# Kernel tuning notes

Measured on AMD Instinct MI355X. Metric: run time of the kernel, lower is better.

Reference implementation:

```python
import jax, jax.numpy as jnp
import numpy as np

TEMPERATURE = 1.0
NEG_INF = -1e30  # finite stand-in for -inf: safe for log_softmax and its vjp


def setup_inputs() -> dict:
    key = jax.random.key(0)
    k1, k2 = jax.random.split(key)
    B, M, D = 4096, 3, 256
    tokens = jax.random.normal(k1, (B, M, D), dtype=jnp.float32)
    labels = jax.random.randint(k2, (B,), 0, 32, dtype=jnp.int32)
    return {"tokens": tokens, "labels": labels}


def reference(tokens, labels):
    # tokens: [B, M, D]; labels: [B]
    B, M, D = tokens.shape
    # Pairwise per-modality similarities: sim[i, k, m] = <tokens[i,m], tokens[k,m]>
    sim = jnp.einsum('imd,kmd->ikm', tokens, tokens) / TEMPERATURE
    self_mask = jnp.eye(B, dtype=bool)
    # Original excludes sample i itself from the candidate set; masking with a
    # huge negative logit makes it contribute 0 to the softmax partition.
    sim = jnp.where(self_mask[:, :, None], NEG_INF, sim)
    logp = jax.nn.log_softmax(sim, axis=1)  # softmax over the B-1 other samples

    # Positive pairs: same label, excluding self.
    pos = (labels[:, None] == labels[None, :]) & ~self_mask  # [B, B]
    pos_count = pos.sum(axis=1)                               # [B]
    valid = pos_count > 0                                     # sum(same_label) > 1

    # Mean log-prob over positives, per (sample, modality).
    pos_logp = jnp.einsum('ikm,ik->im', logp, pos.astype(logp.dtype))  # [B, M]
    denom = jnp.maximum(pos_count, 1).astype(logp.dtype)[:, None]
    per = jnp.where(valid[:, None], pos_logp / denom, 0.0)             # [B, M]

    num = valid.sum() * M
    return -per.sum() / num.astype(per.dtype)
```

## Files before the change

### kernel.cpp

```cpp
#include <hip/hip_runtime.h>

#define B_N 4096
#define M_N 3
#define D_N 256
#define LOG2E 1.44269504088896340736f
#define LN2   0.69314718055994530942f
#define C_OFF   64.0f
#define T_CLAMP 112.0f

typedef __bf16 bf16x8 __attribute__((ext_vector_type(8)));
typedef float  f32x4  __attribute__((ext_vector_type(4)));

__device__ __forceinline__ unsigned short f2bf(float f) {
    unsigned int u = __float_as_uint(f);
    u += 0x7FFFu + ((u >> 16) & 1u);
    return (unsigned short)(u >> 16);
}
__device__ __forceinline__ float bf2f(unsigned short h) {
    return __uint_as_float(((unsigned int)h) << 16);
}

__global__ void cvt_kernel(const float* __restrict__ in, unsigned short* __restrict__ out,
                           float* __restrict__ norm2) {
    int idx = blockIdx.x * blockDim.x + threadIdx.x;
    float4 v = reinterpret_cast<const float4*>(in)[idx];
    int i   = idx / 192;
    int rem = idx - i * 192;
    int m   = rem >> 6;
    int d4  = rem & 63;
    ushort4 o;
    o.x = f2bf(v.x); o.y = f2bf(v.y); o.z = f2bf(v.z); o.w = f2bf(v.w);
    reinterpret_cast<ushort4*>(out)[((size_t)m * B_N + i) * 64 + d4] = o;
    float nx = bf2f(o.x), ny = bf2f(o.y), nz = bf2f(o.z), nw = bf2f(o.w);
    float s = nx * nx + ny * ny + nz * nz + nw * nw;
#pragma unroll
    for (int msk = 1; msk < 64; msk <<= 1) s += __shfl_xor(s, msk);
    if ((threadIdx.x & 63) == 0) norm2[m * B_N + i] = s;
}

__global__ __launch_bounds__(256, 3) void main_kernel(
    const unsigned short* __restrict__ tokb, const int* __restrict__ labels,
    float2* __restrict__ partials) {
    int raw = blockIdx.x;
    int bid = (raw & 7) * 96 + (raw >> 3);
    int m  = bid >> 8;
    int ns = (bid >> 5) & 7;
    int rb = bid & 31;
    int i0 = rb * 128;
    int cb = ns * 512;

    int tid  = threadIdx.x;
    int wave = tid >> 6, lane = tid & 63;
    int lr = lane & 15, lk = lane >> 4;
    const unsigned short* tm = tokb + (size_t)m * (B_N * D_N);

    __shared__ __align__(16) char ldsB[2][8192];
    __shared__ int labl[512];
    labl[tid]       = labels[cb + tid];
    labl[tid + 256] = labels[cb + tid + 256];

    int r0 = i0 + wave * 32;
    bf16x8 afrag[2][8];
#pragma unroll
    for (int rt = 0; rt < 2; ++rt) {
        const unsigned short* rp = tm + (size_t)(r0 + rt * 16 + lr) * D_N + lk * 8;
#pragma unroll
        for (int kf = 0; kf < 8; ++kf)
            afrag[rt][kf] = *reinterpret_cast<const bf16x8*>(rp + kf * 32);
    }
    int labr[2][4];
#pragma unroll
    for (int rt = 0; rt < 2; ++rt)
#pragma unroll
        for (int j = 0; j < 4; ++j)
            labr[rt][j] = labels[r0 + rt * 16 + lk * 4 + j];

    float S[2][4] = {{0.f, 0.f, 0.f, 0.f}, {0.f, 0.f, 0.f, 0.f}};
    float P[2][4] = {{0.f, 0.f, 0.f, 0.f}, {0.f, 0.f, 0.f, 0.f}};

    int lc  = tid >> 5;
    int w   = tid & 31;
    int sch = w ^ (lc & 7);
    const unsigned short* sbase = tm + (size_t)(cb + lc) * D_N + sch * 8;

#define COMPUTE(KB, BUF)                                                            \
    {                                                                               \
        int kb_ = (KB);                                                             \
        const char* bp = ldsB[BUF];                                                 \
        int swz = (lr & 7) << 4;                                                    \
        bf16x8 bfrag[8];                                                            \
        _Pragma("unroll")                                                           \
        for (int kf = 0; kf < 8; ++kf)                                              \
            bfrag[kf] = *reinterpret_cast<const bf16x8*>(                           \
                bp + lr * 512 + (((kf * 4 + lk) << 4) ^ swz));                      \
        int labc = labl[kb_ * 16 + lr];                                             \
        f32x4 acc0 = {0.f, 0.f, 0.f, 0.f};                                          \
        f32x4 acc1 = {0.f, 0.f, 0.f, 0.f};                                          \
        _Pragma("unroll")                                                           \
        for (int kf = 0; kf < 8; ++kf) {                                            \
            acc0 = __builtin_amdgcn_mfma_f32_16x16x32_bf16(afrag[0][kf], bfrag[kf], \
                                                           acc0, 0, 0, 0);          \
            acc1 = __builtin_amdgcn_mfma_f32_16x16x32_bf16(afrag[1][kf], bfrag[kf], \
                                                           acc1, 0, 0, 0);          \
        }                                                                           \
        int cg0 = cb + kb_ * 16;                                                    \
        if ((cg0 < r0 + 32) && (cg0 + 16 > r0)) {                                   \
            int colg = cg0 + lr;                                                    \
            _Pragma("unroll")                                                       \
            for (int rt = 0; rt < 2; ++rt) {                                        \
                f32x4 aa = rt ? acc1 : acc0;                                        \
                _Pragma("unroll")                                                   \
                for (int j = 0; j < 4; ++j) {                                       \
                    float s2 = aa[j];                                               \
                    float t = fminf(fmaf(s2, LOG2E, -C_OFF), T_CLAMP);               \
                    float e = __builtin_amdgcn_exp2f(t);                            \
                    int row = r0 + rt * 16 + lk * 4 + j;                            \
                    e = (colg == row) ? 0.f : e;   \
                    S[rt][j] += e;                                                  \
                    P[rt][j] += (labc == labr[rt][j]) ? s2 : 0.f;                   \
                }                                                                   \
            }                                                                       \
        } else {                                                                    \
            _Pragma("unroll")                                                       \
            for (int rt = 0; rt < 2; ++rt) {                                        \
                f32x4 aa = rt ? acc1 : acc0;                                        \
                _Pragma("unroll")                                                   \
                for (int j = 0; j < 4; ++j) {                                       \
                    float s2 = aa[j];                                               \
                    float t = fminf(fmaf(s2, LOG2E, -C_OFF), T_CLAMP);               \
                    S[rt][j] += __builtin_amdgcn_exp2f(t);                          \
                    P[rt][j] += (labc == labr[rt][j]) ? s2 : 0.f;                   \
                }                                                                   \
            }                                                                       \
        }                                                                           \
    }

    {
        bf16x8 t0 = *reinterpret_cast<const bf16x8*>(sbase);
        bf16x8 t1 = *reinterpret_cast<const bf16x8*>(sbase + 8 * D_N);
        *reinterpret_cast<bf16x8*>(&ldsB[0][tid * 16])        = t0;
        *reinterpret_cast<bf16x8*>(&ldsB[0][4096 + tid * 16]) = t1;
    }
    const unsigned short* p1 = sbase + (size_t)(16 * D_N);
    bf16x8 gA0 = *reinterpret_cast<const bf16x8*>(p1);
    bf16x8 gA1 = *reinterpret_cast<const bf16x8*>(p1 + 8 * D_N);

    for (int it = 0; it < 16; ++it) {
        __syncthreads();
        {
            const unsigned short* np =
                sbase + (size_t)((2 * it + 2) & 31) * (16 * D_N);
            bf16x8 gB0 = *reinterpret_cast<const bf16x8*>(np);
            bf16x8 gB1 = *reinterpret_cast<const bf16x8*>(np + 8 * D_N);
            COMPUTE(2 * it, 0);
            *reinterpret_cast<bf16x8*>(&ldsB[1][tid * 16])        = gA0;
            *reinterpret_cast<bf16x8*>(&ldsB[1][4096 + tid * 16]) = gA1;
            __syncthreads();
            const unsigned short* np2 =
                sbase + (size_t)((2 * it + 3) & 31) * (16 * D_N);
            gA0 = *reinterpret_cast<const bf16x8*>(np2);
            gA1 = *reinterpret_cast<const bf16x8*>(np2 + 8 * D_N);
            COMPUTE(2 * it + 1, 1);
            *reinterpret_cast<bf16x8*>(&ldsB[0][tid * 16])        = gB0;
            *reinterpret_cast<bf16x8*>(&ldsB[0][4096 + tid * 16]) = gB1;
        }
    }
#undef COMPUTE

#pragma unroll
    for (int rt = 0; rt < 2; ++rt)
#pragma unroll
        for (int j = 0; j < 4; ++j) {
            float sv = S[rt][j], pv = P[rt][j];
#pragma unroll
            for (int msk = 1; msk < 16; msk <<= 1) {
                sv += __shfl_xor(sv, msk);
                pv += __shfl_xor(pv, msk);
            }
            if (lr == 0) {
                int rl = rt * 16 + lk * 4 + j;
                float2 q; q.x = sv; q.y = pv;
                partials[(size_t)(((m * 32 + rb) * 8 + ns) * 128) + wave * 32 + rl] = q;
            }
        }
}

__global__ void reduce_kernel(const float2* __restrict__ partials,
                              const float* __restrict__ norm2,
                              const int* __restrict__ labels,
                              float* __restrict__ blockpart,
                              int* __restrict__ nvout) {
    __shared__ int h[32];
    int tid = threadIdx.x;
    if (tid < 32) h[tid] = 0;
    __syncthreads();
    for (int i = tid; i < B_N; i += 256) atomicAdd(&h[labels[i]], 1);
    __syncthreads();
    if (blockIdx.x == 0 && tid == 0) {
        int nv = 0;
#pragma unroll
        for (int c = 0; c < 32; ++c) nv += (h[c] >= 2) ? h[c] : 0;
        nvout[0] = nv;
    }
    int gid = blockIdx.x * 256 + tid;
    int m = gid >> 12, i = gid & 4095;
    int rb = i >> 7, r = i & 127;
    const float2* pp = partials + (size_t)(((m * 32 + rb) * 8) * 128) + r;
    float S = 0.f, P = 0.f;
#pragma unroll
    for (int ns = 0; ns < 8; ++ns) {
        float2 q = pp[ns * 128];
        S += q.x; P += q.y;
    }
    P -= norm2[gid];
    int pc = h[labels[i]] - 1;
    float contrib = (pc > 0)
        ? (__builtin_amdgcn_logf(S) + C_OFF) * LN2 - P / (float)pc
        : 0.f;
#pragma unroll
    for (int off = 32; off >= 1; off >>= 1) contrib += __shfl_down(contrib, off);
    __shared__ float w4[4];
    if ((tid & 63) == 0) w4[tid >> 6] = contrib;
    __syncthreads();
    if (tid == 0) blockpart[blockIdx.x] = w4[0] + w4[1] + w4[2] + w4[3];
}

__global__ void final_kernel(const float* __restrict__ blockpart, const int* __restrict__ nv,
                             float* __restrict__ out) {
    int lane = threadIdx.x;
    float s = (lane < 48) ? blockpart[lane] : 0.f;
#pragma unroll
    for (int off = 32; off >= 1; off >>= 1) s += __shfl_down(s, off);
    if (lane == 0) out[0] = s / (float)(nv[0] * M_N);
}

extern "C" void kernel_launch(void* const* d_in, const int* in_sizes, int n_in,
                              void* d_out, int out_size, void* d_ws, size_t ws_size,
                              hipStream_t stream) {
    const float* tokens = (const float*)d_in[0];
    const int*   labels = (const int*)d_in[1];
    float* out = (float*)d_out;

    char* ws = (char*)d_ws;
    int*    nv        = (int*)(ws + 128);
    float*  blockpart = (float*)(ws + 256);
    float*  norm2     = (float*)(ws + 1024);
    float2* partials  = (float2*)(ws + 65536);
    unsigned short* tokb = (unsigned short*)(ws + 1048576);

    cvt_kernel<<<3072, 256, 0, stream>>>(tokens, tokb, norm2);
    main_kernel<<<768, 256, 0, stream>>>(tokb, labels, partials);
    reduce_kernel<<<48, 256, 0, stream>>>(partials, norm2, labels, blockpart, nv);
    final_kernel<<<1, 64, 0, stream>>>(blockpart, nv, out);
}
```

Before: 58.27 us.

## Triple-buffer LDS and prefetch next B fragments into registers during MFMA

Replaces the double-buffered LDS scheme with a three-slot rotation and register double-buffering of the B fragments, so the next tile's LDS reads overlap the current tile's MFMAs and each phase needs only one barrier. Redundant wrap-around global loads at the tail are skipped. Launch bounds drop from 3 to 2 blocks per CU to leave room for the extra fragment registers, which may lower occupancy and hurt latency hiding.

```diff
diff --git a/kernel.cpp b/kernel.cpp
--- a/kernel.cpp
+++ b/kernel.cpp
@@ -38,7 +38,7 @@
     if ((threadIdx.x & 63) == 0) norm2[m * B_N + i] = s;
 }
 
-__global__ __launch_bounds__(256, 3) void main_kernel(
+__global__ __launch_bounds__(256, 2) void main_kernel(
     const unsigned short* __restrict__ tokb, const int* __restrict__ labels,
     float2* __restrict__ partials) {
     int raw = blockIdx.x;
@@ -54,7 +54,7 @@
     int lr = lane & 15, lk = lane >> 4;
     const unsigned short* tm = tokb + (size_t)m * (B_N * D_N);
 
-    __shared__ __align__(16) char ldsB[2][8192];
+    __shared__ __align__(16) char ldsB[3][8192];
     __shared__ int labl[512];
     labl[tid]       = labels[cb + tid];
     labl[tid + 256] = labels[cb + tid + 256];
@@ -82,90 +82,97 @@
     int w   = tid & 31;
     int sch = w ^ (lc & 7);
     const unsigned short* sbase = tm + (size_t)(cb + lc) * D_N + sch * 8;
-
-#define COMPUTE(KB, BUF)                                                            \
-    {                                                                               \
-        int kb_ = (KB);                                                             \
-        const char* bp = ldsB[BUF];                                                 \
-        int swz = (lr & 7) << 4;                                                    \
-        bf16x8 bfrag[8];                                                            \
-        _Pragma("unroll")                                                           \
-        for (int kf = 0; kf < 8; ++kf)                                              \
-            bfrag[kf] = *reinterpret_cast<const bf16x8*>(                           \
-                bp + lr * 512 + (((kf * 4 + lk) << 4) ^ swz));                      \
-        int labc = labl[kb_ * 16 + lr];                                             \
-        f32x4 acc0 = {0.f, 0.f, 0.f, 0.f};                                          \
-        f32x4 acc1 = {0.f, 0.f, 0.f, 0.f};                                          \
-        _Pragma("unroll")                                                           \
-        for (int kf = 0; kf < 8; ++kf) {                                            \
-            acc0 = __builtin_amdgcn_mfma_f32_16x16x32_bf16(afrag[0][kf], bfrag[kf], \
-                                                           acc0, 0, 0, 0);          \
-            acc1 = __builtin_amdgcn_mfma_f32_16x16x32_bf16(afrag[1][kf], bfrag[kf], \
-                                                           acc1, 0, 0, 0);          \
-        }                                                                           \
-        int cg0 = cb + kb_ * 16;                                                    \
-        if ((cg0 < r0 + 32) && (cg0 + 16 > r0)) {                                   \
-            int colg = cg0 + lr;                                                    \
-            _Pragma("unroll")                                                       \
-            for (int rt = 0; rt < 2; ++rt) {                                        \
-                f32x4 aa = rt ? acc1 : acc0;                                        \
-                _Pragma("unroll")                                                   \
-                for (int j = 0; j < 4; ++j) {                                       \
-                    float s2 = aa[j];                                               \
-                    float t = fminf(fmaf(s2, LOG2E, -C_OFF), T_CLAMP);               \
-                    float e = __builtin_amdgcn_exp2f(t);                            \
-                    int row = r0 + rt * 16 + lk * 4 + j;                            \
-                    e = (colg == row) ? 0.f : e;   \
-                    S[rt][j] += e;                                                  \
-                    P[rt][j] += (labc == labr[rt][j]) ? s2 : 0.f;                   \
-                }                                                                   \
-            }                                                                       \
-        } else {                                                                    \
-            _Pragma("unroll")                                                       \
-            for (int rt = 0; rt < 2; ++rt) {                                        \
-                f32x4 aa = rt ? acc1 : acc0;                                        \
-                _Pragma("unroll")                                                   \
-                for (int j = 0; j < 4; ++j) {                                       \
-                    float s2 = aa[j];                                               \
-                    float t = fminf(fmaf(s2, LOG2E, -C_OFF), T_CLAMP);               \
-                    S[rt][j] += __builtin_amdgcn_exp2f(t);                          \
-                    P[rt][j] += (labc == labr[rt][j]) ? s2 : 0.f;                   \
-                }                                                                   \
-            }                                                                       \
-        }                                                                           \
-    }
+    int swz = (lr & 7) << 4;
 
     {
-        bf16x8 t0 = *reinterpret_cast<const bf16x8*>(sbase);
-        bf16x8 t1 = *reinterpret_cast<const bf16x8*>(sbase + 8 * D_N);
-        *reinterpret_cast<bf16x8*>(&ldsB[0][tid * 16])        = t0;
-        *reinterpret_cast<bf16x8*>(&ldsB[0][4096 + tid * 16]) = t1;
-    }
-    const unsigned short* p1 = sbase + (size_t)(16 * D_N);
-    bf16x8 gA0 = *reinterpret_cast<const bf16x8*>(p1);
-    bf16x8 gA1 = *reinterpret_cast<const bf16x8*>(p1 + 8 * D_N);
+        bf16x8 a0 = *reinterpret_cast<const bf16x8*>(sbase);
+        bf16x8 a1 = *reinterpret_cast<const bf16x8*>(sbase + 8 * D_N);
+        bf16x8 b0 = *reinterpret_cast<const bf16x8*>(sbase + 16 * D_N);
+        bf16x8 b1 = *reinterpret_cast<const bf16x8*>(sbase + 24 * D_N);
+        *reinterpret_cast<bf16x8*>(&ldsB[0][tid * 16])        = a0;
+        *reinterpret_cast<bf16x8*>(&ldsB[0][4096 + tid * 16]) = a1;
+        *reinterpret_cast<bf16x8*>(&ldsB[1][tid * 16])        = b0;
+        *reinterpret_cast<bf16x8*>(&ldsB[1][4096 + tid * 16]) = b1;
+    }
+    __syncthreads();
+
+    char* pc = ldsB[0];
+    char* pn = ldsB[1];
+    char* ps = ldsB[2];
+
+    bf16x8 bfA[8], bfB[8];
+#pragma unroll
+    for (int kf = 0; kf < 8; ++kf)
+        bfA[kf] = *reinterpret_cast<const bf16x8*>(pc + lr * 512 + (((kf * 4 + lk) << 4) ^ swz));
+
+#define PHASE(KB, BFC, BFN)                                                          \
+    {                                                                                \
+        int kb_ = (KB);                                                              \
+        bf16x8 nt0, nt1;                                                             \
+        if (kb_ < 30) {                \
+            const unsigned short* np = sbase + (size_t)(kb_ + 2) * (16 * D_N);       \
+            nt0 = *reinterpret_cast<const bf16x8*>(np);                              \
+            nt1 = *reinterpret_cast<const bf16x8*>(np + 8 * D_N);                    \
+        }                                                                            \
+        f32x4 acc0 = {0.f, 0.f, 0.f, 0.f};                                           \
+        f32x4 acc1 = {0.f, 0.f, 0.f, 0.f};                                           \
+        _Pragma("unroll")                                                            \
+        for (int kf = 0; kf < 8; ++kf) {                                             \
+            acc0 = __builtin_amdgcn_mfma_f32_16x16x32_bf16(afrag[0][kf], BFC[kf],    \
+                                                           acc0, 0, 0, 0);           \
+            acc1 = __builtin_amdgcn_mfma_f32_16x16x32_bf16(afrag[1][kf], BFC[kf],    \
+                                                           acc1, 0, 0, 0);           \
+        }                                                                            \
+        if (kb_ < 31) {      \
+            _Pragma("unroll")                                                        \
+            for (int kf = 0; kf < 8; ++kf)                                           \
+                BFN[kf] = *reinterpret_cast<const bf16x8*>(                          \
+                    pn + lr * 512 + (((kf * 4 + lk) << 4) ^ swz));                   \
+        }                                                                            \
+        int labc = labl[kb_ * 16 + lr];                                              \
+        int cg0 = cb + kb_ * 16;                                                     \
+        if ((cg0 < r0 + 32) && (cg0 + 16 > r0)) {                                    \
+            int colg = cg0 + lr;                                                     \
+            _Pragma("unroll")                                                        \
+            for (int rt = 0; rt < 2; ++rt) {                                         \
+                f32x4 aa = rt ? acc1 : acc0;                                         \
+                _Pragma("unroll")                                                    \
+                for (int j = 0; j < 4; ++j) {                                        \
+                    float s2 = aa[j];                                                \
+                    float t = fminf(fmaf(s2, LOG2E, -C_OFF), T_CLAMP);                \
+                    float e = __builtin_amdgcn_exp2f(t);                             \
+                    int row = r0 + rt * 16 + lk * 4 + j;                             \
+                    e = (colg == row) ? 0.f : e;                                     \
+                    S[rt][j] += e;                                                   \
+                    P[rt][j] += (labc == labr[rt][j]) ? s2 : 0.f;                    \
+                }                                                                    \
+            }                                                                        \
+        } else {                                                                     \
+            _Pragma("unroll")                                                        \
+            for (int rt = 0; rt < 2; ++rt) {                                         \
+                f32x4 aa = rt ? acc1 : acc0;                                         \
+                _Pragma("unroll")                                                    \
+                for (int j = 0; j < 4; ++j) {                                        \
+                    float s2 = aa[j];                                                \
+                    float t = fminf(fmaf(s2, LOG2E, -C_OFF), T_CLAMP);                \
+                    S[rt][j] += __builtin_amdgcn_exp2f(t);                           \
+                    P[rt][j] += (labc == labr[rt][j]) ? s2 : 0.f;                    \
+                }                                                                    \
+            }                                                                        \
+        }                                                                            \
+        if (kb_ < 30) {                                         \
+            *reinterpret_cast<bf16x8*>(ps + tid * 16)        = nt0;                  \
+            *reinterpret_cast<bf16x8*>(ps + 4096 + tid * 16) = nt1;                  \
+        }                                                                            \
+        __syncthreads();                                                             \
+        char* tmp_ = pc; pc = pn; pn = ps; ps = tmp_;                                \
+    }
 
     for (int it = 0; it < 16; ++it) {
-        __syncthreads();
-        {
-            const unsigned short* np =
-                sbase + (size_t)((2 * it + 2) & 31) * (16 * D_N);
-            bf16x8 gB0 = *reinterpret_cast<const bf16x8*>(np);
-            bf16x8 gB1 = *reinterpret_cast<const bf16x8*>(np + 8 * D_N);
-            COMPUTE(2 * it, 0);
-            *reinterpret_cast<bf16x8*>(&ldsB[1][tid * 16])        = gA0;
-            *reinterpret_cast<bf16x8*>(&ldsB[1][4096 + tid * 16]) = gA1;
-            __syncthreads();
-            const unsigned short* np2 =
-                sbase + (size_t)((2 * it + 3) & 31) * (16 * D_N);
-            gA0 = *reinterpret_cast<const bf16x8*>(np2);
-            gA1 = *reinterpret_cast<const bf16x8*>(np2 + 8 * D_N);
-            COMPUTE(2 * it + 1, 1);
-            *reinterpret_cast<bf16x8*>(&ldsB[0][tid * 16])        = gB0;
-            *reinterpret_cast<bf16x8*>(&ldsB[0][4096 + tid * 16]) = gB1;
-        }
-    }
-#undef COMPUTE
+        PHASE(2 * it,     bfA, bfB);
+        PHASE(2 * it + 1, bfB, bfA);
+    }
+#undef PHASE
 
 #pragma unroll
     for (int rt = 0; rt < 2; ++rt)
```

Result: faster. 54.89 us (-5.8%).

## Exploit Gram matrix symmetry by computing only upper-triangular tiles

Applied to the files above, without the earlier changes.

Each (modality, 128x128 block-pair) tile in the upper triangle is now computed once. Its exp-sums and positive-similarity sums feed both the row samples and, for off-diagonal tiles, the column samples through per-column shared-memory reductions. Results are accumulated with global atomics into a zeroed per-sample buffer, replacing the partials array, so the reduce kernel reads a single value per row. This roughly halves the MFMA and exp work, at the cost of extra column shuffles, LDS traffic, atomics and a memset.

```diff
diff --git a/kernel.cpp b/kernel.cpp
--- a/kernel.cpp
+++ b/kernel.cpp
@@ -40,14 +40,16 @@
 
 __global__ __launch_bounds__(256, 3) void main_kernel(
     const unsigned short* __restrict__ tokb, const int* __restrict__ labels,
-    float2* __restrict__ partials) {
+    float* __restrict__ gacc) {
     int raw = blockIdx.x;
-    int bid = (raw & 7) * 96 + (raw >> 3);
-    int m  = bid >> 8;
-    int ns = (bid >> 5) & 7;
-    int rb = bid & 31;
-    int i0 = rb * 128;
-    int cb = ns * 512;
+    int bid = (raw & 7) * 198 + (raw >> 3);
+    int m    = bid / 528;
+    int beta = bid - m * 528;
+    int b = 0;
+    while ((b + 1) * (b + 2) / 2 <= beta) ++b;
+    int a = beta - (b * (b + 1)) / 2;
+    bool offd = (a != b);
+    int cb = b * 128;
 
     int tid  = threadIdx.x;
     int wave = tid >> 6, lane = tid & 63;
@@ -55,11 +57,11 @@
     const unsigned short* tm = tokb + (size_t)m * (B_N * D_N);
 
     __shared__ __align__(16) char ldsB[2][8192];
-    __shared__ int labl[512];
-    labl[tid]       = labels[cb + tid];
-    labl[tid + 256] = labels[cb + tid + 256];
-
-    int r0 = i0 + wave * 32;
+    __shared__ int labl[128];
+    __shared__ float colbuf[4][8][16][2];
+    if (tid < 128) labl[tid] = labels[cb + tid];
+
+    int r0 = a * 128 + wave * 32;
     bf16x8 afrag[2][8];
 #pragma unroll
     for (int rt = 0; rt < 2; ++rt) {
@@ -83,17 +85,30 @@
     int sch = w ^ (lc & 7);
     const unsigned short* sbase = tm + (size_t)(cb + lc) * D_N + sch * 8;
 
-#define COMPUTE(KB, BUF)                                                            \
+    {
+        bf16x8 t0 = *reinterpret_cast<const bf16x8*>(sbase);
+        bf16x8 t1 = *reinterpret_cast<const bf16x8*>(sbase + 8 * D_N);
+        *reinterpret_cast<bf16x8*>(&ldsB[0][tid * 16])        = t0;
+        *reinterpret_cast<bf16x8*>(&ldsB[0][4096 + tid * 16]) = t1;
+    }
+
+#define PHASE(KB)                                                                   \
     {                                                                               \
-        int kb_ = (KB);                                                             \
-        const char* bp = ldsB[BUF];                                                 \
+        __syncthreads();       \
+        bf16x8 nt0, nt1;                                                            \
+        if (KB < 7) {                                                               \
+            const unsigned short* np = sbase + (size_t)(KB + 1) * (16 * D_N);       \
+            nt0 = *reinterpret_cast<const bf16x8*>(np);                             \
+            nt1 = *reinterpret_cast<const bf16x8*>(np + 8 * D_N);                   \
+        }                                                                           \
+        const char* bp = ldsB[KB & 1];                                              \
         int swz = (lr & 7) << 4;                                                    \
         bf16x8 bfrag[8];                                                            \
         _Pragma("unroll")                                                           \
         for (int kf = 0; kf < 8; ++kf)                                              \
             bfrag[kf] = *reinterpret_cast<const bf16x8*>(                           \
                 bp + lr * 512 + (((kf * 4 + lk) << 4) ^ swz));                      \
-        int labc = labl[kb_ * 16 + lr];                                             \
+        int labc = labl[KB * 16 + lr];                                              \
         f32x4 acc0 = {0.f, 0.f, 0.f, 0.f};                                          \
         f32x4 acc1 = {0.f, 0.f, 0.f, 0.f};                                          \
         _Pragma("unroll")                                                           \
@@ -103,8 +118,9 @@
             acc1 = __builtin_amdgcn_mfma_f32_16x16x32_bf16(afrag[1][kf], bfrag[kf], \
                                                            acc1, 0, 0, 0);          \
         }                                                                           \
-        int cg0 = cb + kb_ * 16;                                                    \
-        if ((cg0 < r0 + 32) && (cg0 + 16 > r0)) {                                   \
+        float cs = 0.f, cp = 0.f;                                                   \
+        int cg0 = cb + KB * 16;                                                     \
+        if ((cg0 < r0 + 32) && (cg0 + 16 > r0)) {          \
             int colg = cg0 + lr;                                                    \
             _Pragma("unroll")                                                       \
             for (int rt = 0; rt < 2; ++rt) {                                        \
@@ -116,8 +132,9 @@
                     float e = __builtin_amdgcn_exp2f(t);                            \
                     int row = r0 + rt * 16 + lk * 4 + j;                            \
                     e = (colg == row) ? 0.f : e;   \
-                    S[rt][j] += e;                                                  \
-                    P[rt][j] += (labc == labr[rt][j]) ? s2 : 0.f;                   \
+                    bool mt = (labc == labr[rt][j]);                                \
+                    S[rt][j] += e;  P[rt][j] += mt ? s2 : 0.f;                      \
+                    cs += e;        cp += mt ? s2 : 0.f;                            \
                 }                                                                   \
             }                                                                       \
         } else {                                                                    \
@@ -128,44 +145,28 @@
                 for (int j = 0; j < 4; ++j) {                                       \
                     float s2 = aa[j];                                               \
                     float t = fminf(fmaf(s2, LOG2E, -C_OFF), T_CLAMP);               \
-                    S[rt][j] += __builtin_amdgcn_exp2f(t);                          \
-                    P[rt][j] += (labc == labr[rt][j]) ? s2 : 0.f;                   \
+                    float e = __builtin_amdgcn_exp2f(t);                            \
+                    bool mt = (labc == labr[rt][j]);                                \
+                    S[rt][j] += e;  P[rt][j] += mt ? s2 : 0.f;                      \
+                    cs += e;        cp += mt ? s2 : 0.f;                            \
                 }                                                                   \
             }                                                                       \
         }                                                                           \
-    }
-
-    {
-        bf16x8 t0 = *reinterpret_cast<const bf16x8*>(sbase);
-        bf16x8 t1 = *reinterpret_cast<const bf16x8*>(sbase + 8 * D_N);
-        *reinterpret_cast<bf16x8*>(&ldsB[0][tid * 16])        = t0;
-        *reinterpret_cast<bf16x8*>(&ldsB[0][4096 + tid * 16]) = t1;
-    }
-    const unsigned short* p1 = sbase + (size_t)(16 * D_N);
-    bf16x8 gA0 = *reinterpret_cast<const bf16x8*>(p1);
-    bf16x8 gA1 = *reinterpret_cast<const bf16x8*>(p1 + 8 * D_N);
-
-    for (int it = 0; it < 16; ++it) {
-        __syncthreads();
-        {
-            const unsigned short* np =
-                sbase + (size_t)((2 * it + 2) & 31) * (16 * D_N);
-            bf16x8 gB0 = *reinterpret_cast<const bf16x8*>(np);
-            bf16x8 gB1 = *reinterpret_cast<const bf16x8*>(np + 8 * D_N);
-            COMPUTE(2 * it, 0);
-            *reinterpret_cast<bf16x8*>(&ldsB[1][tid * 16])        = gA0;
-            *reinterpret_cast<bf16x8*>(&ldsB[1][4096 + tid * 16]) = gA1;
-            __syncthreads();
-            const unsigned short* np2 =
-                sbase + (size_t)((2 * it + 3) & 31) * (16 * D_N);
-            gA0 = *reinterpret_cast<const bf16x8*>(np2);
-            gA1 = *reinterpret_cast<const bf16x8*>(np2 + 8 * D_N);
-            COMPUTE(2 * it + 1, 1);
-            *reinterpret_cast<bf16x8*>(&ldsB[0][tid * 16])        = gB0;
-            *reinterpret_cast<bf16x8*>(&ldsB[0][4096 + tid * 16]) = gB1;
-        }
-    }
-#undef COMPUTE
+                           \
+        cs += __shfl_xor(cs, 16); cs += __shfl_xor(cs, 32);                         \
+        cp += __shfl_xor(cp, 16); cp += __shfl_xor(cp, 32);                         \
+        if (lk == 0) { colbuf[wave][KB][lr][0] = cs; colbuf[wave][KB][lr][1] = cp; }\
+        if (KB < 7) {                                                               \
+            char* dst = (char*)ldsB[(KB & 1) ^ 1];                                  \
+            *reinterpret_cast<bf16x8*>(dst + tid * 16)        = nt0;                \
+            *reinterpret_cast<bf16x8*>(dst + 4096 + tid * 16) = nt1;                \
+        }                                                                           \
+    }
+
+    PHASE(0) PHASE(1) PHASE(2) PHASE(3) PHASE(4) PHASE(5) PHASE(6) PHASE(7)
+#undef PHASE
+
+    __syncthreads();
 
 #pragma unroll
     for (int rt = 0; rt < 2; ++rt)
@@ -178,14 +179,27 @@
                 pv += __shfl_xor(pv, msk);
             }
             if (lr == 0) {
-                int rl = rt * 16 + lk * 4 + j;
-                float2 q; q.x = sv; q.y = pv;
-                partials[(size_t)(((m * 32 + rb) * 8 + ns) * 128) + wave * 32 + rl] = q;
+                int row = r0 + rt * 16 + lk * 4 + j;
+                float* g = gacc + (size_t)(m * B_N + row) * 2;
+                atomicAdd(g, sv);
+                atomicAdd(g + 1, pv);
             }
         }
-}
-
-__global__ void reduce_kernel(const float2* __restrict__ partials,
+
+    if (offd && tid < 128) {
+        int kb = tid >> 4, cr = tid & 15;
+        float sv = colbuf[0][kb][cr][0] + colbuf[1][kb][cr][0]
+                 + colbuf[2][kb][cr][0] + colbuf[3][kb][cr][0];
+        float pv = colbuf[0][kb][cr][1] + colbuf[1][kb][cr][1]
+                 + colbuf[2][kb][cr][1] + colbuf[3][kb][cr][1];
+        int col = cb + tid;
+        float* g = gacc + (size_t)(m * B_N + col) * 2;
+        atomicAdd(g, sv);
+        atomicAdd(g + 1, pv);
+    }
+}
+
+__global__ void reduce_kernel(const float* __restrict__ gacc,
                               const float* __restrict__ norm2,
                               const int* __restrict__ labels,
                               float* __restrict__ blockpart,
@@ -203,16 +217,9 @@
         nvout[0] = nv;
     }
     int gid = blockIdx.x * 256 + tid;
-    int m = gid >> 12, i = gid & 4095;
-    int rb = i >> 7, r = i & 127;
-    const float2* pp = partials + (size_t)(((m * 32 + rb) * 8) * 128) + r;
-    float S = 0.f, P = 0.f;
-#pragma unroll
-    for (int ns = 0; ns < 8; ++ns) {
-        float2 q = pp[ns * 128];
-        S += q.x; P += q.y;
-    }
-    P -= norm2[gid];
+    int i = gid & 4095;
+    float S = gacc[(size_t)gid * 2];
+    float P = gacc[(size_t)gid * 2 + 1] - norm2[gid];
     int pc = h[labels[i]] - 1;
     float contrib = (pc > 0)
         ? (__builtin_amdgcn_logf(S) + C_OFF) * LN2 - P / (float)pc
@@ -245,11 +252,12 @@
     int*    nv        = (int*)(ws + 128);
     float*  blockpart = (float*)(ws + 256);
     float*  norm2     = (float*)(ws + 1024);
-    float2* partials  = (float2*)(ws + 65536);
+    float*  gacc      = (float*)(ws + 65536);
     unsigned short* tokb = (unsigned short*)(ws + 1048576);
 
+    hipMemsetAsync(gacc, 0, 12288 * 2 * sizeof(float), stream);
     cvt_kernel<<<3072, 256, 0, stream>>>(tokens, tokb, norm2);
-    main_kernel<<<768, 256, 0, stream>>>(tokb, labels, partials);
-    reduce_kernel<<<48, 256, 0, stream>>>(partials, norm2, labels, blockpart, nv);
+    main_kernel<<<1584, 256, 0, stream>>>(tokb, labels, gacc);
+    reduce_kernel<<<48, 256, 0, stream>>>(gacc, norm2, labels, blockpart, nv);
     final_kernel<<<1, 64, 0, stream>>>(blockpart, nv, out);
 }
```

New measurement: 89.97 us. 1.54x slower.
